# Kernel tuning notes

Measured on AMD Instinct MI355X. Metric: run time of the kernel, lower is better.

## Reference

```python
import jax, jax.numpy as jnp
import numpy as np

D = 768      # activation_dim
F = 16384    # dict_size
K = 64       # top-k
B = 4096     # batch of activation vectors


def setup_inputs() -> dict:
    key = jax.random.key(0)
    k1, k2, k3 = jax.random.split(key, 3)
    x = jax.random.normal(k1, (B, D), dtype=jnp.float32)
    W_enc = jax.random.normal(k2, (F, D), dtype=jnp.float32) * 0.02
    b_enc = jnp.zeros((F,), dtype=jnp.float32)
    W_dec = jax.random.normal(k3, (D, F), dtype=jnp.float32)
    # decoder columns normalized to unit norm (set_decoder_norm_to_unit_norm)
    eps = jnp.finfo(jnp.float32).eps
    W_dec = W_dec / (jnp.linalg.norm(W_dec, axis=0, keepdims=True) + eps)
    b_dec = jnp.zeros((D,), dtype=jnp.float32)
    return {"x": x, "W_enc": W_enc, "b_enc": b_enc, "W_dec": W_dec, "b_dec": b_dec}


def reference(x, W_enc, b_enc, W_dec, b_dec):
    # encode: pre_activation_BF = encoder(x - b_dec)
    pre_BF = jnp.einsum('bd,fd->bf', x - b_dec, W_enc) + b_enc
    # top-k selection along feature dim
    vals_BK, idx_BK = jax.lax.top_k(pre_BF, K)
    # scatter top-k values into sparse code buffer [B, F]
    rows = jnp.arange(pre_BF.shape[0])[:, None]
    f_BF = jnp.zeros_like(pre_BF).at[rows, idx_BK].set(vals_BK)
    # decode: x_hat = decoder(f) + b_dec
    x_hat_BD = jnp.einsum('bf,df->bd', f_BF, W_dec) + b_dec
    return x_hat_BD
```

## Files before the change

### kernel.cpp

```cpp
#include <hip/hip_runtime.h>
#include <cstdint>
#include <cstddef>

#define Dd 768
#define Ff 16384
#define Bb 4096
#define Kk 64
#define NCAND 128
#define BINS 512
#define MARGIN 0.04f

typedef __bf16 bf16x8 __attribute__((ext_vector_type(8)));
typedef float  f32x4  __attribute__((ext_vector_type(4)));
typedef unsigned short u16x8 __attribute__((ext_vector_type(8)));

__device__ __forceinline__ unsigned short f2bf(float f) {
    union { float f; unsigned u; } a; a.f = f;
    unsigned r = a.u + 0x7fffu + ((a.u >> 16) & 1u);
    return (unsigned short)(r >> 16);
}
__device__ __forceinline__ float bf2f(unsigned short h) {
    union { float f; unsigned u; } a; a.u = ((unsigned)h) << 16;
    return a.f;
}
__device__ __forceinline__ float f_lo(unsigned u) {
    union { float f; unsigned u; } a; a.u = u << 16; return a.f;
}
__device__ __forceinline__ float f_hi(unsigned u) {
    union { float f; unsigned u; } a; a.u = u & 0xffff0000u; return a.f;
}

#define GLDS16(g, l) __builtin_amdgcn_global_load_lds( \
    (const __attribute__((address_space(1))) void*)(g), \
    (__attribute__((address_space(3))) void*)(l), 16, 0, 0)

__global__ __launch_bounds__(256) void conv_x(
    const float* __restrict__ x, const float* __restrict__ bdec,
    unsigned short* __restrict__ Xb)
{
    const int i = blockIdx.x * 256 + threadIdx.x;
    const int col = i % Dd;
    Xb[i] = f2bf(x[i] - bdec[col]);
}

__global__ __launch_bounds__(256) void conv_w(
    const float* __restrict__ Wenc, unsigned short* __restrict__ Wb)
{
    const int i = blockIdx.x * 256 + threadIdx.x;
    Wb[i] = f2bf(Wenc[i]);
}

__global__ __launch_bounds__(512, 2) void sae_gemm(
    const unsigned short* __restrict__ Xb,
    const unsigned short* __restrict__ Wb,
    const float* __restrict__ benc,
    unsigned short* __restrict__ pre)
{
    __shared__ __align__(16) unsigned short As[32768];
    __shared__ __align__(16) unsigned short Bs[32768];

    const int tid  = threadIdx.x;
    const int lane = tid & 63;
    const int w    = tid >> 6;
    const int wm   = w >> 2, wn = w & 3;

    const int bid = blockIdx.x;
    const int wg  = (bid & 7) * 128 + (bid >> 3);
    const int n0  = (wg & 63) * 256;
    const int m0  = (wg >> 6) * 256;

    const int r0 = tid >> 2,           r1 = (512 + tid) >> 2;
    const int q0 = (tid - (tid >> 3)) & 3;
    const int q1 = ((512 + tid) - ((512 + tid) >> 3)) & 3;
    const unsigned short* aS0 = Xb + (size_t)(m0 + r0) * Dd + q0 * 8;
    const unsigned short* aS1 = Xb + (size_t)(m0 + r1) * Dd + q1 * 8;
    const unsigned short* bS0 = Wb + (size_t)(n0 + r0) * Dd + q0 * 8;
    const unsigned short* bS1 = Wb + (size_t)(n0 + r1) * Dd + q1 * 8;
    unsigned short* lA = As + w * 512;
    unsigned short* lB = Bs + w * 512;

    const int rl  = lane & 15;
    const int rot = ((lane >> 4) + (rl >> 1)) & 3;
    const unsigned asO = (unsigned)(unsigned long long)
        (__attribute__((address_space(3))) unsigned short*)&As[0];
    const unsigned bsO = (unsigned)(unsigned long long)
        (__attribute__((address_space(3))) unsigned short*)&Bs[0];
    const unsigned aRd = asO + (unsigned)((wm * 128 + rl) * 64 + rot * 16);
    const unsigned bRd = bsO + (unsigned)((wn * 64 + rl) * 64 + rot * 16);

    f32x4 acc[8][4];
    #pragma unroll
    for (int i = 0; i < 8; ++i)
        #pragma unroll
        for (int j = 0; j < 4; ++j) acc[i][j] = 0;

#define DSR(D, A) asm volatile("ds_read_b128 %0, %1" : "=v"(D) : "v"(A))
#define STG1(MS0, MS1, LDSB, TILE, KH, BUF) {                                 \
    GLDS16(MS0 + (TILE) * 64 + (KH) * 32,                                     \
           LDSB + (BUF) * 16384 + (KH) * 8192);                               \
    GLDS16(MS1 + (TILE) * 64 + (KH) * 32,                                     \
           LDSB + (BUF) * 16384 + (KH) * 8192 + 4096); }
#define STAGE_G(TILE, KH, BUF) { STG1(aS0, aS1, lA, TILE, KH, BUF);           \
                                 STG1(bS0, bS1, lB, TILE, KH, BUF); }
#define VM8 asm volatile("s_waitcnt vmcnt(8)" ::: "memory")

#define MF1(H, MI, NI) acc[(H)*4+(MI)][(NI)] =                                \
    __builtin_amdgcn_mfma_f32_16x16x32_bf16(                                  \
        __builtin_bit_cast(bf16x8, af[(MI)]),                                 \
        __builtin_bit_cast(bf16x8, bfr[(NI)]), acc[(H)*4+(MI)][(NI)], 0, 0, 0)
#define MFQ(H)                                                                \
    MF1(H,0,0); MF1(H,0,1); MF1(H,0,2); MF1(H,0,3);                           \
    MF1(H,1,0); MF1(H,1,1); MF1(H,1,2); MF1(H,1,3);                           \
    MF1(H,2,0); MF1(H,2,1); MF1(H,2,2); MF1(H,2,3);                           \
    MF1(H,3,0); MF1(H,3,1); MF1(H,3,2); MF1(H,3,3)

#define PH(BUF, KH, H, STAGE_STMT, VM_STMT) {                                 \
    f32x4 af[4];                                                              \
    const unsigned ab = aRd + (BUF)*32768 + (KH)*16384 + (H)*4096;            \
    DSR(af[0], ab);        DSR(af[1], ab + 1024);                             \
    DSR(af[2], ab + 2048); DSR(af[3], ab + 3072);                             \
    if ((H) == 0) {                                                           \
        const unsigned bb = bRd + (BUF)*32768 + (KH)*16384;                   \
        DSR(bfr[0], bb);        DSR(bfr[1], bb + 1024);                       \
        DSR(bfr[2], bb + 2048); DSR(bfr[3], bb + 3072);                       \
    }                                                                         \
    STAGE_STMT;                                                               \
    __builtin_amdgcn_s_barrier();                                             \
    asm volatile("s_waitcnt lgkmcnt(0)" ::: "memory");                        \
    __builtin_amdgcn_sched_barrier(0);                                        \
    __builtin_amdgcn_s_setprio(1);                                            \
    MFQ(H);                                                                   \
    __builtin_amdgcn_s_setprio(0);                                            \
    VM_STMT;                                                                  \
    __builtin_amdgcn_s_barrier(); }

    STAGE_G(0, 0, 0);
    STAGE_G(0, 1, 0);
    STAGE_G(1, 0, 1);
    asm volatile("s_waitcnt vmcnt(8)" ::: "memory");
    __builtin_amdgcn_s_barrier();

    f32x4 bfr[4];
    for (int i = 0; i < 6; ++i) {
        const int t1 = 2 * i + 1, t2 = 2 * i + 2, t3 = 2 * i + 3;
        PH(0, 0, 0, STAGE_G(t1, 1, 1), (void)0);
        PH(0, 0, 1, (void)0,           VM8);
        PH(0, 1, 0, STAGE_G(t2, 0, 0), (void)0);
        PH(0, 1, 1, (void)0,           VM8);
        PH(1, 0, 0, STAGE_G(t2, 1, 0), (void)0);
        PH(1, 0, 1, (void)0,           VM8);
        PH(1, 1, 0, STAGE_G(t3, 0, 1), (void)0);
        PH(1, 1, 1, (void)0,           VM8);
    }

    const int cl = lane & 15;
    const int rb = (lane >> 4) * 4;
    #pragma unroll
    for (int ni = 0; ni < 4; ++ni) {
        const int ccol = n0 + wn * 64 + ni * 16 + cl;
        const float bia = benc[ccol];
        #pragma unroll
        for (int mi = 0; mi < 8; ++mi) {
            const int row = m0 + wm * 128 + mi * 16 + rb;
            #pragma unroll
            for (int j = 0; j < 4; ++j)
                pre[(size_t)(row + j) * Ff + ccol] = f2bf(acc[mi][ni][j] + bia);
        }
    }
    asm volatile("s_waitcnt vmcnt(0)" ::: "memory");

#undef DSR
#undef STG1
#undef STAGE_G
#undef VM8
#undef MF1
#undef MFQ
#undef PH
}

__global__ __launch_bounds__(256) void sae_select(
    const unsigned short* __restrict__ pre,
    int* __restrict__ ci, int* __restrict__ ccount)
{
    __shared__ unsigned hist[2][BINS];
    __shared__ float tauS[2];
    __shared__ int lcnt[2];

    const int tid = threadIdx.x;
    const int r   = tid >> 7;
    const int l   = tid & 127;
    const int rg  = blockIdx.x * 2 + r;

    for (int i = tid; i < 2 * BINS; i += 256) ((unsigned*)hist)[i] = 0;
    if (tid < 2) lcnt[tid] = 0;
    __syncthreads();

    const u16x8* rp = (const u16x8*)(pre + (size_t)rg * Ff);
    for (int j = 0; j < 16; ++j) {
        const u16x8 v8 = rp[j * 128 + l];
        #pragma unroll
        for (int c = 0; c < 8; ++c) {
            const float v = bf2f(v8[c]);
            if (v >= 0.0f) {
                const int b = min((int)(v * 128.0f), BINS - 1);
                atomicAdd(&hist[r][b], 1u);
            }
        }
    }
    __syncthreads();

    if (l == 0) {
        unsigned acc = 0; float tv = -1.0e30f;
        for (int j = BINS - 1; j >= 0; --j) {
            acc += hist[r][j];
            if (acc >= (unsigned)Kk) { tv = (float)j * 0.0078125f; break; }
        }
        tauS[r] = tv;
    }
    __syncthreads();

    const float thr = tauS[r] - MARGIN;
    for (int j = 0; j < 16; ++j) {
        const u16x8 v8 = rp[j * 128 + l];
        #pragma unroll
        for (int c = 0; c < 8; ++c) {
            const float v = bf2f(v8[c]);
            if (v >= thr) {
                const int p = atomicAdd(&lcnt[r], 1);
                if (p < NCAND) ci[(size_t)rg * NCAND + p] = j * 1024 + l * 8 + c;
            }
        }
    }
    __syncthreads();
    if (l == 0) ccount[rg] = min(lcnt[r], NCAND);
}

__global__ __launch_bounds__(256) void sae_rescore(
    const float* __restrict__ x, const float* __restrict__ Wenc,
    const float* __restrict__ benc, const float* __restrict__ bdec,
    const int* __restrict__ ci, const int* __restrict__ ccount,
    float* __restrict__ ovals, int* __restrict__ oidx)
{
    __shared__ float  xr[Dd];
    __shared__ int    cis[NCAND];
    __shared__ double es[NCAND];
    __shared__ int    cnt;

    const int r = blockIdx.x, tid = threadIdx.x;
    const int lane = tid & 63, w = tid >> 6;

    xr[tid]       = x[(size_t)r * Dd + tid]       - bdec[tid];
    xr[tid + 256] = x[(size_t)r * Dd + tid + 256] - bdec[tid + 256];
    xr[tid + 512] = x[(size_t)r * Dd + tid + 512] - bdec[tid + 512];
    if (tid == 0) cnt = ccount[r];
    if (tid < NCAND) cis[tid] = ci[(size_t)r * NCAND + tid];
    if (tid < Kk) { ovals[(size_t)r * Kk + tid] = 0.0f; oidx[(size_t)r * Kk + tid] = 0; }
    __syncthreads();

    for (int c = w; c < NCAND; c += 4) {
        double e = -1.0e300;
        if (c < cnt) {
            const int f = cis[c];
            const float* wrow = Wenc + (size_t)f * Dd;
            double a = 0.0;
            #pragma unroll
            for (int j = 0; j < Dd / 64; ++j)
                a = fma((double)wrow[j * 64 + lane], (double)xr[j * 64 + lane], a);
            #pragma unroll
            for (int off = 32; off > 0; off >>= 1)
                a += __shfl_xor(a, off);
            e = a + (double)benc[f];
        }
        if (lane == 0) es[c] = e;
    }
    __syncthreads();

    if (tid < NCAND) {
        const double e = es[tid];
        int rk = 0;
        for (int j = 0; j < NCAND; ++j) {
            const double ej = es[j];
            rk += (ej > e) || (ej == e && j < tid);
        }
        if (tid < cnt && rk < Kk) {
            ovals[(size_t)r * Kk + rk] = (float)e;
            oidx [(size_t)r * Kk + rk] = cis[tid];
        }
    }
}

__global__ __launch_bounds__(256) void sae_transpose(
    const float* __restrict__ Wd, unsigned short* __restrict__ WdT)
{
    __shared__ float tile[32][33];
    const int f0 = blockIdx.x * 32;
    const int d0 = blockIdx.y * 32;
    const int tx = threadIdx.x, ty = threadIdx.y;
    #pragma unroll
    for (int k = 0; k < 4; ++k)
        tile[ty + 8 * k][tx] = Wd[(size_t)(d0 + ty + 8 * k) * Ff + f0 + tx];
    __syncthreads();
    #pragma unroll
    for (int k = 0; k < 4; ++k)
        WdT[(size_t)(f0 + ty + 8 * k) * Dd + d0 + tx] = f2bf(tile[tx][ty + 8 * k]);
}

__global__ __launch_bounds__(192) void sae_decode(
    const unsigned short* __restrict__ WdT, const float* __restrict__ vals,
    const int* __restrict__ idx, const float* __restrict__ bdec,
    float* __restrict__ out)
{
    __shared__ float sv[Kk];
    __shared__ int   si[Kk];
    const int b = blockIdx.x, tid = threadIdx.x;
    if (tid < Kk) { sv[tid] = vals[(size_t)b * Kk + tid]; si[tid] = idx[(size_t)b * Kk + tid]; }
    __syncthreads();
    const int d0 = tid * 4;
    float a0 = bdec[d0], a1 = bdec[d0 + 1], a2 = bdec[d0 + 2], a3 = bdec[d0 + 3];
    for (int k = 0; k < Kk; ++k) {
        const float v = sv[k];
        const uint2 p = *(const uint2*)(WdT + (size_t)si[k] * Dd + d0);
        a0 = fmaf(v, f_lo(p.x), a0);
        a1 = fmaf(v, f_hi(p.x), a1);
        a2 = fmaf(v, f_lo(p.y), a2);
        a3 = fmaf(v, f_hi(p.y), a3);
    }
    float4 o4 = make_float4(a0, a1, a2, a3);
    *(float4*)(out + (size_t)b * Dd + d0) = o4;
}

extern "C" void kernel_launch(void* const* d_in, const int* in_sizes, int n_in,
                              void* d_out, int out_size, void* d_ws, size_t ws_size,
                              hipStream_t stream) {
    const float* x    = (const float*)d_in[0];
    const float* Wenc = (const float*)d_in[1];
    const float* benc = (const float*)d_in[2];
    const float* Wdec = (const float*)d_in[3];
    const float* bdec = (const float*)d_in[4];
    float* out = (float*)d_out;

    char* ws = (char*)d_ws;
    size_t o = 0;
    unsigned short* pre  = (unsigned short*)(ws + o); o += (size_t)Bb * Ff * 2;
    unsigned short* Xb   = (unsigned short*)(ws + o); o += (size_t)Bb * Dd * 2;
    unsigned short* Wb   = (unsigned short*)(ws + o); o += (size_t)Ff * Dd * 2;
    unsigned short* WdT  = (unsigned short*)(ws + o); o += (size_t)Ff * Dd * 2;
    int*            cib  = (int*)(ws + o);            o += (size_t)Bb * NCAND * 4;
    int*            ccnt = (int*)(ws + o);            o += (size_t)Bb * 4;
    float*          vals = (float*)(ws + o);          o += (size_t)Bb * Kk * 4;
    int*            idxb = (int*)(ws + o);

    conv_x<<<(Bb * Dd) / 256, 256, 0, stream>>>(x, bdec, Xb);
    conv_w<<<(Ff * Dd) / 256, 256, 0, stream>>>(Wenc, Wb);
    sae_gemm<<<(Bb / 256) * (Ff / 256), 512, 0, stream>>>(Xb, Wb, benc, pre);
    sae_select<<<Bb / 2, 256, 0, stream>>>(pre, cib, ccnt);
    sae_rescore<<<Bb, 256, 0, stream>>>(x, Wenc, benc, bdec, cib, ccnt, vals, idxb);
    sae_transpose<<<dim3(Ff / 32, Dd / 32), dim3(32, 8), 0, stream>>>(Wdec, WdT);
    sae_decode<<<Bb, 192, 0, stream>>>(WdT, vals, idxb, bdec, out);
}
```

Before: 553.6 us.

## Halve GEMM LDS tiles, simplify double-buffer pipeline, vectorize transposed epilogue stores

The encoder GEMM now stages 32-wide K tiles instead of 64-wide ones. This halves LDS use, and launch bounds request 4 blocks per CU instead of 2. The pipeline becomes a plain two-buffer loop with vmcnt(4) waits, and the workgroup-to-tile mapping groups 8 N-tiles per XCD for L2 reuse. MFMA operands are swapped so each lane holds 4 consecutive columns, which lets the bias add and bf16 stores be packed into 8-byte writes. The trade-off is more barriers per K step and a higher occupancy target that may not fit within the register budget.

```diff
diff --git a/kernel.cpp b/kernel.cpp
--- a/kernel.cpp
+++ b/kernel.cpp
@@ -50,14 +50,14 @@
     Wb[i] = f2bf(Wenc[i]);
 }
 
-__global__ __launch_bounds__(512, 2) void sae_gemm(
+__global__ __launch_bounds__(512, 4) void sae_gemm(
     const unsigned short* __restrict__ Xb,
     const unsigned short* __restrict__ Wb,
     const float* __restrict__ benc,
     unsigned short* __restrict__ pre)
 {
-    __shared__ __align__(16) unsigned short As[32768];
-    __shared__ __align__(16) unsigned short Bs[32768];
+    __shared__ __align__(16) unsigned short As[16384];
+    __shared__ __align__(16) unsigned short Bs[16384];
 
     const int tid  = threadIdx.x;
     const int lane = tid & 63;
@@ -65,9 +65,10 @@
     const int wm   = w >> 2, wn = w & 3;
 
     const int bid = blockIdx.x;
-    const int wg  = (bid & 7) * 128 + (bid >> 3);
-    const int n0  = (wg & 63) * 256;
-    const int m0  = (wg >> 6) * 256;
+    const int xcd = bid & 7;
+    const int c   = bid >> 3;
+    const int n0  = (xcd * 8 + (c & 7)) * 256;
+    const int m0  = (c >> 3) * 256;
 
     const int r0 = tid >> 2,           r1 = (512 + tid) >> 2;
     const int q0 = (tid - (tid >> 3)) & 3;
@@ -95,84 +96,85 @@
         for (int j = 0; j < 4; ++j) acc[i][j] = 0;
 
 #define DSR(D, A) asm volatile("ds_read_b128 %0, %1" : "=v"(D) : "v"(A))
-#define STG1(MS0, MS1, LDSB, TILE, KH, BUF) {                                 \
-    GLDS16(MS0 + (TILE) * 64 + (KH) * 32,                                     \
-           LDSB + (BUF) * 16384 + (KH) * 8192);                               \
-    GLDS16(MS1 + (TILE) * 64 + (KH) * 32,                                     \
-           LDSB + (BUF) * 16384 + (KH) * 8192 + 4096); }
-#define STAGE_G(TILE, KH, BUF) { STG1(aS0, aS1, lA, TILE, KH, BUF);           \
-                                 STG1(bS0, bS1, lB, TILE, KH, BUF); }
-#define VM8 asm volatile("s_waitcnt vmcnt(8)" ::: "memory")
+#define STG(TILE, BUF) {                                                      \
+    GLDS16(aS0 + (TILE) * 32, lA + (BUF) * 8192);                             \
+    GLDS16(aS1 + (TILE) * 32, lA + (BUF) * 8192 + 4096);                      \
+    GLDS16(bS0 + (TILE) * 32, lB + (BUF) * 8192);                             \
+    GLDS16(bS1 + (TILE) * 32, lB + (BUF) * 8192 + 4096); }
+#define VM4 asm volatile("s_waitcnt vmcnt(4)" ::: "memory")
+#define VM0 asm volatile("s_waitcnt vmcnt(0)" ::: "memory")
 
 #define MF1(H, MI, NI) acc[(H)*4+(MI)][(NI)] =                                \
     __builtin_amdgcn_mfma_f32_16x16x32_bf16(                                  \
-        __builtin_bit_cast(bf16x8, af[(MI)]),                                 \
-        __builtin_bit_cast(bf16x8, bfr[(NI)]), acc[(H)*4+(MI)][(NI)], 0, 0, 0)
+        __builtin_bit_cast(bf16x8, bfr[(NI)]),                                \
+        __builtin_bit_cast(bf16x8, af[(MI)]), acc[(H)*4+(MI)][(NI)], 0, 0, 0)
 #define MFQ(H)                                                                \
     MF1(H,0,0); MF1(H,0,1); MF1(H,0,2); MF1(H,0,3);                           \
     MF1(H,1,0); MF1(H,1,1); MF1(H,1,2); MF1(H,1,3);                           \
     MF1(H,2,0); MF1(H,2,1); MF1(H,2,2); MF1(H,2,3);                           \
     MF1(H,3,0); MF1(H,3,1); MF1(H,3,2); MF1(H,3,3)
 
-#define PH(BUF, KH, H, STAGE_STMT, VM_STMT) {                                 \
+#define PH(BUF, H) {                                                          \
     f32x4 af[4];                                                              \
-    const unsigned ab = aRd + (BUF)*32768 + (KH)*16384 + (H)*4096;            \
+    const unsigned ab = aRd + (BUF)*16384 + (H)*4096;                         \
     DSR(af[0], ab);        DSR(af[1], ab + 1024);                             \
     DSR(af[2], ab + 2048); DSR(af[3], ab + 3072);                             \
     if ((H) == 0) {                                                           \
-        const unsigned bb = bRd + (BUF)*32768 + (KH)*16384;                   \
+        const unsigned bb = bRd + (BUF)*16384;                                \
         DSR(bfr[0], bb);        DSR(bfr[1], bb + 1024);                       \
         DSR(bfr[2], bb + 2048); DSR(bfr[3], bb + 3072);                       \
     }                                                                         \
-    STAGE_STMT;                                                               \
     __builtin_amdgcn_s_barrier();                                             \
     asm volatile("s_waitcnt lgkmcnt(0)" ::: "memory");                        \
     __builtin_amdgcn_sched_barrier(0);                                        \
     __builtin_amdgcn_s_setprio(1);                                            \
     MFQ(H);                                                                   \
     __builtin_amdgcn_s_setprio(0);                                            \
-    VM_STMT;                                                                  \
     __builtin_amdgcn_s_barrier(); }
 
-    STAGE_G(0, 0, 0);
-    STAGE_G(0, 1, 0);
-    STAGE_G(1, 0, 1);
-    asm volatile("s_waitcnt vmcnt(8)" ::: "memory");
+    STG(0, 0);
+    STG(1, 1);
+    VM4;
     __builtin_amdgcn_s_barrier();
 
     f32x4 bfr[4];
-    for (int i = 0; i < 6; ++i) {
-        const int t1 = 2 * i + 1, t2 = 2 * i + 2, t3 = 2 * i + 3;
-        PH(0, 0, 0, STAGE_G(t1, 1, 1), (void)0);
-        PH(0, 0, 1, (void)0,           VM8);
-        PH(0, 1, 0, STAGE_G(t2, 0, 0), (void)0);
-        PH(0, 1, 1, (void)0,           VM8);
-        PH(1, 0, 0, STAGE_G(t2, 1, 0), (void)0);
-        PH(1, 0, 1, (void)0,           VM8);
-        PH(1, 1, 0, STAGE_G(t3, 0, 1), (void)0);
-        PH(1, 1, 1, (void)0,           VM8);
-    }
-
-    const int cl = lane & 15;
-    const int rb = (lane >> 4) * 4;
-    #pragma unroll
-    for (int ni = 0; ni < 4; ++ni) {
-        const int ccol = n0 + wn * 64 + ni * 16 + cl;
-        const float bia = benc[ccol];
+    for (int t = 0; t < 22; t += 2) {
+        PH(0, 0); PH(0, 1);
+        STG(t + 2, 0); VM4; __builtin_amdgcn_s_barrier();
+        PH(1, 0); PH(1, 1);
+        STG(t + 3, 1); VM4; __builtin_amdgcn_s_barrier();
+    }
+    PH(0, 0); PH(0, 1);
+    VM0; __builtin_amdgcn_s_barrier();
+    PH(1, 0); PH(1, 1);
+
+    const int rl2  = lane & 15;
+    const int cg   = (lane >> 4) * 4;
+    const int colb = n0 + wn * 64;
+    float4 bia[4];
+    #pragma unroll
+    for (int ni = 0; ni < 4; ++ni)
+        bia[ni] = *(const float4*)&benc[colb + ni * 16 + cg];
+    #pragma unroll
+    for (int mi = 0; mi < 8; ++mi) {
+        const int row = m0 + wm * 128 + mi * 16 + rl2;
+        unsigned short* prow = pre + (size_t)row * Ff + colb;
         #pragma unroll
-        for (int mi = 0; mi < 8; ++mi) {
-            const int row = m0 + wm * 128 + mi * 16 + rb;
-            #pragma unroll
-            for (int j = 0; j < 4; ++j)
-                pre[(size_t)(row + j) * Ff + ccol] = f2bf(acc[mi][ni][j] + bia);
-        }
-    }
-    asm volatile("s_waitcnt vmcnt(0)" ::: "memory");
+        for (int ni = 0; ni < 4; ++ni) {
+            const f32x4 a = acc[mi][ni];
+            uint2 pk;
+            pk.x = (unsigned)f2bf(a[0] + bia[ni].x)
+                 | ((unsigned)f2bf(a[1] + bia[ni].y) << 16);
+            pk.y = (unsigned)f2bf(a[2] + bia[ni].z)
+                 | ((unsigned)f2bf(a[3] + bia[ni].w) << 16);
+            *(uint2*)(prow + ni * 16 + cg) = pk;
+        }
+    }
 
 #undef DSR
-#undef STG1
-#undef STAGE_G
-#undef VM8
+#undef STG
+#undef VM4
+#undef VM0
 #undef MF1
 #undef MFQ
 #undef PH
```

Result: slower. 1.455 ms (+162.9%).
